# Kernel optimization log

Hardware: AMD Instinct MI355X
Metric: run time of the kernel (lower is better)

## Reference

```python
import jax, jax.numpy as jnp
import numpy as np

S, F, K, D, H, DT = 64, 10, 7, 512, 14, 128


def _mlp(x, W1, b1, W2, b2, g, b):
    # Linear(512,128) -> ReLU -> Linear(128,128) -> BatchNorm1d(128) (eval mode = affine)
    h = jax.nn.relu(x @ W1 + b1)
    y = h @ W2 + b2
    return y * g + b


def setup_inputs() -> dict:
    key = jax.random.key(0)
    ks = jax.random.split(key, 10)
    rng = np.random.default_rng(0)
    # per-(seg,class) random frame permutation and random class picks (torch.randperm / randint)
    perm_idx = jnp.asarray(np.argsort(rng.random((S, K, F)), axis=-1), jnp.int32)
    cls_idx = jnp.asarray(rng.integers(0, K, (S, K, F)), jnp.int32)
    sc = 0.02
    return {
        "feat_a": jax.random.normal(ks[0], (S, K, D), jnp.float32),
        "pred_a": jax.random.uniform(ks[1], (S, K), jnp.float32),
        "feat_v_raw": jax.random.normal(ks[2], (S * F, D, H, H), jnp.float32),
        "pred_v": jax.random.normal(ks[3], (S * F, K), jnp.float32),
        "cam": jax.random.uniform(ks[4], (S * F, K, H, H), jnp.float32),
        "W1a": jax.random.normal(ks[5], (D, DT), jnp.float32) * sc,
        "b1a": jnp.zeros((DT,), jnp.float32),
        "W2a": jax.random.normal(ks[6], (DT, DT), jnp.float32) * sc,
        "b2a": jnp.zeros((DT,), jnp.float32),
        "ga": jnp.ones((DT,), jnp.float32),
        "bna": jnp.zeros((DT,), jnp.float32),
        "W1v": jax.random.normal(ks[7], (D, DT), jnp.float32) * sc,
        "b1v": jnp.zeros((DT,), jnp.float32),
        "W2v": jax.random.normal(ks[8], (DT, DT), jnp.float32) * sc,
        "b2v": jnp.zeros((DT,), jnp.float32),
        "gv": jnp.ones((DT,), jnp.float32),
        "bnv": jnp.zeros((DT,), jnp.float32),
        "perm_idx": perm_idx,
        "cls_idx": cls_idx,
    }


def reference(feat_a, pred_a, feat_v_raw, pred_v, cam,
              W1a, b1a, W2a, b2a, ga, bna,
              W1v, b1v, W2v, b2v, gv, bnv,
              perm_idx, cls_idx):
    # cam-weighted foreground pooling (cam_pool fg branch), contracted so the
    # [N,K,D,HW] intermediate is never materialized
    cam_sum = jnp.sum(cam, axis=(-2, -1)) + 1e-10            # [N,K]
    fg = jnp.einsum('nchw,nkhw->nkc', feat_v_raw, cam) / cam_sum[..., None]
    feat_v = fg.reshape(S, F, K, D)                           # [S,F,K,D]

    pv = jax.nn.sigmoid(pred_v).reshape(S, F, K)              # index_v

    Ta = _mlp(feat_a, W1a, b1a, W2a, b2a, ga, bna)            # [S,K,DT]
    Tv = _mlp(feat_v, W1v, b1v, W2v, b2v, gv, bnv)            # [S,F,K,DT]

    # 'same' pairs: (seg, class k, frame f) with pred_a>0.3 and sigmoid(pred_v)>0.3
    Tvt = jnp.transpose(Tv, (0, 2, 1, 3))                     # [S,K,F,DT]
    loss_co = jnp.mean((Ta[:, :, None, :] - Tvt) ** 2, -1)    # [S,K,F]

    # 'differ' pairs: partner segment rank = seg^1, random frame perm + random class,
    # first num = floor(pred_a*F) entries kept
    rank = jnp.arange(S) ^ 1
    Tv_d = Tv[rank[:, None, None], perm_idx, cls_idx]         # [S,K,F,DT]
    loss_di = jnp.mean((Ta[:, :, None, :] - Tv_d) ** 2, -1)   # [S,K,F]

    act_a = pred_a > 0.3                                      # index_a
    num = jnp.floor(pred_a * F).astype(jnp.int32)
    mask_co = act_a[:, :, None] & (jnp.transpose(pv, (0, 2, 1)) > 0.3)
    mask_di = act_a[:, :, None] & (jnp.arange(F)[None, None, :] < num[:, :, None])

    losses = jnp.stack([loss_co * mask_co, loss_di * mask_di], 0)  # [2,S,K,F]
    return losses, mask_co, mask_di
```

## Files before the change

kernel.cpp:

```cpp
#include <hip/hip_runtime.h>
#include <hip/hip_bf16.h>
#include <math.h>

#define S 64
#define F 10
#define K 7
#define D 512
#define HH 196
#define DT 128
#define NF (S*F)
#define NROWS_V (S*F*K)
#define NROWS_A (S*K)
#define NOUT (S*K*F)
#define MLP_R 8
#define NA_BLK (NROWS_A / MLP_R)
#define NV_BLK (NROWS_V / MLP_R)
#define WT 32
#define WTILE_F4 (WT * DT / 4)

typedef short bf16x8 __attribute__((ext_vector_type(8)));
typedef float f32x4 __attribute__((ext_vector_type(4)));

__device__ __forceinline__ short bfc(float x) {
  __hip_bfloat16 h = __float2bfloat16(x);
  return *reinterpret_cast<short*>(&h);
}

__global__ __launch_bounds__(256) void fg_kernel(
    const float* __restrict__ feat, const float* __restrict__ cam,
    float* __restrict__ fg) {
  const int t = threadIdx.x;
  const int lane = t & 63;
  const int w = t >> 6;
  const int col = lane & 15;
  const int kg = lane >> 4;
  const int n = blockIdx.x >> 1;
  const int half = blockIdx.x & 1;
  const int c0blk = half * 256;

  const float* featn = feat + ((size_t)n * D + c0blk) * HH;
  const float* camn = cam + (size_t)n * K * HH;

  bf16x8 bs[7];
  {
    const float* crow = camn + col * HH;
#pragma unroll
    for (int s = 0; s < 7; ++s) {
      float v0 = 0.f, v1 = 0.f, v2 = 0.f, v3 = 0.f;
      float v4 = 0.f, v5 = 0.f, v6 = 0.f, v7 = 0.f;
      if (col < 7) {
        if (s < 6) {
          const float4 lo = *reinterpret_cast<const float4*>(crow + s * 32 + kg * 8);
          const float4 hi = *reinterpret_cast<const float4*>(crow + s * 32 + kg * 8 + 4);
          v0 = lo.x; v1 = lo.y; v2 = lo.z; v3 = lo.w;
          v4 = hi.x; v5 = hi.y; v6 = hi.z; v7 = hi.w;
        } else if (kg == 0) {
          const float4 lo = *reinterpret_cast<const float4*>(crow + 192);
          v0 = lo.x; v1 = lo.y; v2 = lo.z; v3 = lo.w;
        }
      }
      bs[s][0] = bfc(v0); bs[s][1] = bfc(v1); bs[s][2] = bfc(v2); bs[s][3] = bfc(v3);
      bs[s][4] = bfc(v4); bs[s][5] = bfc(v5); bs[s][6] = bfc(v6); bs[s][7] = bfc(v7);
    }
  }

  float invc = 0.f;
#pragma unroll
  for (int k = 0; k < K; ++k) {
    float4 cv = (lane < 49)
                    ? *reinterpret_cast<const float4*>(camn + k * HH + 4 * lane)
                    : make_float4(0.f, 0.f, 0.f, 0.f);
    float s = cv.x + cv.y + cv.z + cv.w;
#pragma unroll
    for (int m = 32; m >= 1; m >>= 1) s += __shfl_xor(s, m, 64);
    const float iv = 1.0f / (s + 1e-10f);
    if (col == k) invc = iv;
  }

  float* fgn = fg + (size_t)n * K * D;

#pragma unroll
  for (int mt = 0; mt < 4; ++mt) {
    const int chl = (w * 4 + mt) * 16 + col;
    const float* rowp = featn + (size_t)chl * HH;

    f32x4 acc = {0.f, 0.f, 0.f, 0.f};
#pragma unroll
    for (int s = 0; s < 7; ++s) {
      float v0 = 0.f, v1 = 0.f, v2 = 0.f, v3 = 0.f;
      float v4 = 0.f, v5 = 0.f, v6 = 0.f, v7 = 0.f;
      if (s < 6) {
        const float4 lo = *reinterpret_cast<const float4*>(rowp + s * 32 + kg * 8);
        const float4 hi = *reinterpret_cast<const float4*>(rowp + s * 32 + kg * 8 + 4);
        v0 = lo.x; v1 = lo.y; v2 = lo.z; v3 = lo.w;
        v4 = hi.x; v5 = hi.y; v6 = hi.z; v7 = hi.w;
      } else if (kg == 0) {
        const float4 lo = *reinterpret_cast<const float4*>(rowp + 192);
        v0 = lo.x; v1 = lo.y; v2 = lo.z; v3 = lo.w;
      }
      bf16x8 a;
      a[0] = bfc(v0); a[1] = bfc(v1); a[2] = bfc(v2); a[3] = bfc(v3);
      a[4] = bfc(v4); a[5] = bfc(v5); a[6] = bfc(v6); a[7] = bfc(v7);
      acc = __builtin_amdgcn_mfma_f32_16x16x32_bf16(a, bs[s], acc, 0, 0, 0);
    }

    if (col < 7) {
      float4 o;
      o.x = acc[0] * invc; o.y = acc[1] * invc;
      o.z = acc[2] * invc; o.w = acc[3] * invc;
      *reinterpret_cast<float4*>(
          fgn + (size_t)col * D + c0blk + (w * 4 + mt) * 16 + kg * 4) = o;
    }
  }
}

__device__ __forceinline__ void fma4(float4& acc, float sx, const float4& wv) {
  acc.x += sx * wv.x; acc.y += sx * wv.y; acc.z += sx * wv.z; acc.w += sx * wv.w;
}

__device__ __forceinline__ void stage_w(const float* src, float4* dst, int t) {
#pragma unroll
  for (int i = 0; i < WTILE_F4; i += 256) {
    __builtin_amdgcn_global_load_lds(
        (const __attribute__((address_space(1))) void*)(src + (size_t)(i + t) * 4),
        (__attribute__((address_space(3))) void*)(dst + i + t), 16, 0, 0);
  }
}

__global__ __launch_bounds__(256) void mlp2_kernel(
    const float* __restrict__ Xa, const float* __restrict__ Xv,
    const float* __restrict__ W1a, const float* __restrict__ b1a,
    const float* __restrict__ W2a, const float* __restrict__ b2a,
    const float* __restrict__ ga, const float* __restrict__ bna,
    const float* __restrict__ W1v, const float* __restrict__ b1v,
    const float* __restrict__ W2v, const float* __restrict__ b2v,
    const float* __restrict__ gv, const float* __restrict__ bnv,
    float* __restrict__ Ta, float* __restrict__ Tv) {
  __shared__ float4 wbuf[2][WTILE_F4];
  __shared__ float hs[MLP_R * DT];
  const int t = threadIdx.x;
  const int b = blockIdx.x;

  const float *X, *W1, *b1, *W2, *b2, *g, *bn;
  float* out;
  int r0;
  if (b < NA_BLK) {
    X = Xa; W1 = W1a; b1 = b1a; W2 = W2a; b2 = b2a; g = ga; bn = bna;
    out = Ta; r0 = b * MLP_R;
  } else {
    X = Xv; W1 = W1v; b1 = b1v; W2 = W2v; b2 = b2v; g = gv; bn = bnv;
    out = Tv; r0 = (b - NA_BLK) * MLP_R;
  }

  const int cg = t & 31;
  const int j0 = cg * 4;
  const int rp = t >> 5;
  const float4* xrow = reinterpret_cast<const float4*>(X + (size_t)(r0 + rp) * D);

  stage_w(W1, &wbuf[0][0], t);
  __syncthreads();

  float4 a0 = *reinterpret_cast<const float4*>(b1 + j0);
  for (int dt = 0; dt < 16; ++dt) {
    if (dt < 15) stage_w(W1 + (size_t)(dt + 1) * WT * DT, &wbuf[(dt + 1) & 1][0], t);
    else         stage_w(W2, &wbuf[0][0], t);
    const float4* wb = &wbuf[dt & 1][0];
#pragma unroll
    for (int d4 = 0; d4 < 8; ++d4) {
      const float4 x0 = xrow[dt * 8 + d4];
      const float4 w0 = wb[(d4 * 4 + 0) * 32 + cg];
      const float4 w1 = wb[(d4 * 4 + 1) * 32 + cg];
      const float4 w2 = wb[(d4 * 4 + 2) * 32 + cg];
      const float4 w3 = wb[(d4 * 4 + 3) * 32 + cg];
      fma4(a0, x0.x, w0); fma4(a0, x0.y, w1); fma4(a0, x0.z, w2); fma4(a0, x0.w, w3);
    }
    __syncthreads();
  }

  a0.x = fmaxf(a0.x, 0.f); a0.y = fmaxf(a0.y, 0.f);
  a0.z = fmaxf(a0.z, 0.f); a0.w = fmaxf(a0.w, 0.f);
  *reinterpret_cast<float4*>(hs + rp * DT + j0) = a0;
  __syncthreads();

  const float4* hrow = reinterpret_cast<const float4*>(hs + rp * DT);

  float4 c0 = *reinterpret_cast<const float4*>(b2 + j0);
  for (int dt = 0; dt < 4; ++dt) {
    if (dt < 3) stage_w(W2 + (size_t)(dt + 1) * WT * DT, &wbuf[(dt + 1) & 1][0], t);
    const float4* wb = &wbuf[dt & 1][0];
#pragma unroll
    for (int d4 = 0; d4 < 8; ++d4) {
      const float4 x0 = hrow[dt * 8 + d4];
      const float4 w0 = wb[(d4 * 4 + 0) * 32 + cg];
      const float4 w1 = wb[(d4 * 4 + 1) * 32 + cg];
      const float4 w2 = wb[(d4 * 4 + 2) * 32 + cg];
      const float4 w3 = wb[(d4 * 4 + 3) * 32 + cg];
      fma4(c0, x0.x, w0); fma4(c0, x0.y, w1); fma4(c0, x0.z, w2); fma4(c0, x0.w, w3);
    }
    __syncthreads();
  }

  const float4 gvv = *reinterpret_cast<const float4*>(g + j0);
  const float4 bv = *reinterpret_cast<const float4*>(bn + j0);
  float4 o0;
  o0.x = c0.x * gvv.x + bv.x; o0.y = c0.y * gvv.y + bv.y;
  o0.z = c0.z * gvv.z + bv.z; o0.w = c0.w * gvv.w + bv.w;
  *reinterpret_cast<float4*>(out + (size_t)(r0 + rp) * DT + j0) = o0;
}

__global__ __launch_bounds__(256) void loss_kernel(
    const float* __restrict__ Ta, const float* __restrict__ Tv,
    const float* __restrict__ pred_a, const float* __restrict__ pred_v,
    const int* __restrict__ perm_idx, const int* __restrict__ cls_idx,
    float* __restrict__ out) {
  const int t = threadIdx.x;
  const int sub = t & 31;
  const int idx = blockIdx.x * 8 + (t >> 5);
  const int f = idx % F;
  const int k = (idx / F) % K;
  const int s = idx / (K * F);

  const int p = perm_idx[idx];
  const int c = cls_idx[idx];
  const int rowd = ((s ^ 1) * F + p) * K + c;

  float4 ta = reinterpret_cast<const float4*>(Ta)[(s * K + k) * 32 + sub];
  float4 tv = reinterpret_cast<const float4*>(Tv)[((s * F + f) * K + k) * 32 + sub];
  float4 td = reinterpret_cast<const float4*>(Tv)[rowd * 32 + sub];
  float d1 = 0.f, d2 = 0.f, e;
  e = ta.x - tv.x; d1 += e * e;
  e = ta.y - tv.y; d1 += e * e;
  e = ta.z - tv.z; d1 += e * e;
  e = ta.w - tv.w; d1 += e * e;
  e = ta.x - td.x; d2 += e * e;
  e = ta.y - td.y; d2 += e * e;
  e = ta.z - td.z; d2 += e * e;
  e = ta.w - td.w; d2 += e * e;
#pragma unroll
  for (int m = 16; m >= 1; m >>= 1) {
    d1 += __shfl_xor(d1, m, 64);
    d2 += __shfl_xor(d2, m, 64);
  }
  if (sub == 0) {
    float pa = pred_a[s * K + k];
    bool act = pa > 0.3f;
    int num = (int)floorf(pa * (float)F);
    float pvv = pred_v[(s * F + f) * K + k];
    float sg = 1.0f / (1.0f + expf(-pvv));
    bool mco = act && (sg > 0.3f);
    bool mdi = act && (f < num);
    float lco = d1 * (1.0f / 128.0f);
    float ldi = d2 * (1.0f / 128.0f);
    out[idx] = mco ? lco : 0.0f;
    out[NOUT + idx] = mdi ? ldi : 0.0f;
    out[2 * NOUT + idx] = mco ? 1.0f : 0.0f;
    out[3 * NOUT + idx] = mdi ? 1.0f : 0.0f;
  }
}

extern "C" void kernel_launch(void* const* d_in, const int* in_sizes, int n_in,
                              void* d_out, int out_size, void* d_ws, size_t ws_size,
                              hipStream_t stream) {
  const float* feat_a     = (const float*)d_in[0];
  const float* pred_a     = (const float*)d_in[1];
  const float* feat_v_raw = (const float*)d_in[2];
  const float* pred_v     = (const float*)d_in[3];
  const float* cam        = (const float*)d_in[4];
  const float* W1a = (const float*)d_in[5];
  const float* b1a = (const float*)d_in[6];
  const float* W2a = (const float*)d_in[7];
  const float* b2a = (const float*)d_in[8];
  const float* ga  = (const float*)d_in[9];
  const float* bna = (const float*)d_in[10];
  const float* W1v = (const float*)d_in[11];
  const float* b1v = (const float*)d_in[12];
  const float* W2v = (const float*)d_in[13];
  const float* b2v = (const float*)d_in[14];
  const float* gv  = (const float*)d_in[15];
  const float* bnv = (const float*)d_in[16];
  const int* perm_idx = (const int*)d_in[17];
  const int* cls_idx  = (const int*)d_in[18];
  float* out = (float*)d_out;

  float* ws = (float*)d_ws;
  float* fg = ws;
  float* Ta = fg + (size_t)NF * K * D;
  float* Tv = Ta + (size_t)NROWS_A * DT;

  fg_kernel<<<NF * 2, 256, 0, stream>>>(feat_v_raw, cam, fg);
  mlp2_kernel<<<NA_BLK + NV_BLK, 256, 0, stream>>>(
      feat_a, fg, W1a, b1a, W2a, b2a, ga, bna,
      W1v, b1v, W2v, b2v, gv, bnv, Ta, Tv);
  loss_kernel<<<NOUT / 8, 256, 0, stream>>>(Ta, Tv, pred_a, pred_v, perm_idx,
                                            cls_idx, out);
}
```

Measured before the change: 82.53 us.

## Run projection MLPs on bf16 MFMA with pre-transposed bf16 weights

Swaps the fp32 FMA MLP kernel, which staged weights through LDS, for an MFMA-based kernel working on 16-row tiles with bf16 inputs. A new conversion kernel casts feat_a to bf16 and transposes and casts the weight matrices each call. fg_kernel now writes its pooled features as bf16, which halves that intermediate's traffic. This adds an extra launch and lowers precision for the MLP inputs and hidden activations.

```diff
diff --git a/kernel.cpp b/kernel.cpp
--- a/kernel.cpp
+++ b/kernel.cpp
@@ -12,23 +12,56 @@
 #define NROWS_V (S*F*K)
 #define NROWS_A (S*K)
 #define NOUT (S*K*F)
-#define MLP_R 8
-#define NA_BLK (NROWS_A / MLP_R)
-#define NV_BLK (NROWS_V / MLP_R)
-#define WT 32
-#define WTILE_F4 (WT * DT / 4)
+#define MLP_BLK_A (NROWS_A / 16)
+#define MLP_BLK_V (NROWS_V / 16)
 
 typedef short bf16x8 __attribute__((ext_vector_type(8)));
 typedef float f32x4 __attribute__((ext_vector_type(4)));
 
-__device__ __forceinline__ short bfc(float x) {
+__device__ __forceinline__ unsigned short bfc(float x) {
   __hip_bfloat16 h = __float2bfloat16(x);
-  return *reinterpret_cast<short*>(&h);
+  return *reinterpret_cast<unsigned short*>(&h);
+}
+
+__global__ __launch_bounds__(256) void conv_kernel(
+    const float* __restrict__ feat_a,
+    const float* __restrict__ W1a, const float* __restrict__ W1v,
+    const float* __restrict__ W2a, const float* __restrict__ W2v,
+    unsigned short* __restrict__ XaB,
+    unsigned short* __restrict__ W1aT, unsigned short* __restrict__ W1vT,
+    unsigned short* __restrict__ W2aT, unsigned short* __restrict__ W2vT) {
+  const int b = blockIdx.x;
+  const int t = threadIdx.x;
+  if (b < 224) {
+    const int o = b * 256 + t;
+    const float4 v = reinterpret_cast<const float4*>(feat_a)[o];
+    unsigned short s0 = bfc(v.x), s1 = bfc(v.y), s2 = bfc(v.z), s3 = bfc(v.w);
+    uint2 pk;
+    pk.x = ((unsigned)s1 << 16) | s0;
+    pk.y = ((unsigned)s3 << 16) | s2;
+    reinterpret_cast<uint2*>(XaB)[o] = pk;
+  } else if (b < 480) {
+    const int o = (b - 224) * 256 + t;
+    const int j = o >> 9, d = o & 511;
+    W1aT[o] = bfc(W1a[d * DT + j]);
+  } else if (b < 736) {
+    const int o = (b - 480) * 256 + t;
+    const int j = o >> 9, d = o & 511;
+    W1vT[o] = bfc(W1v[d * DT + j]);
+  } else if (b < 800) {
+    const int o = (b - 736) * 256 + t;
+    const int j = o >> 7, d = o & 127;
+    W2aT[o] = bfc(W2a[d * DT + j]);
+  } else {
+    const int o = (b - 800) * 256 + t;
+    const int j = o >> 7, d = o & 127;
+    W2vT[o] = bfc(W2v[d * DT + j]);
+  }
 }
 
 __global__ __launch_bounds__(256) void fg_kernel(
     const float* __restrict__ feat, const float* __restrict__ cam,
-    float* __restrict__ fg) {
+    unsigned short* __restrict__ fgb) {
   const int t = threadIdx.x;
   const int lane = t & 63;
   const int w = t >> 6;
@@ -77,7 +110,7 @@
     if (col == k) invc = iv;
   }
 
-  float* fgn = fg + (size_t)n * K * D;
+  unsigned short* fgn = fgb + (size_t)n * K * D;
 
 #pragma unroll
   for (int mt = 0; mt < 4; ++mt) {
@@ -105,107 +138,99 @@
     }
 
     if (col < 7) {
-      float4 o;
-      o.x = acc[0] * invc; o.y = acc[1] * invc;
-      o.z = acc[2] * invc; o.w = acc[3] * invc;
-      *reinterpret_cast<float4*>(
-          fgn + (size_t)col * D + c0blk + (w * 4 + mt) * 16 + kg * 4) = o;
-    }
-  }
-}
-
-__device__ __forceinline__ void fma4(float4& acc, float sx, const float4& wv) {
-  acc.x += sx * wv.x; acc.y += sx * wv.y; acc.z += sx * wv.z; acc.w += sx * wv.w;
-}
-
-__device__ __forceinline__ void stage_w(const float* src, float4* dst, int t) {
-#pragma unroll
-  for (int i = 0; i < WTILE_F4; i += 256) {
-    __builtin_amdgcn_global_load_lds(
-        (const __attribute__((address_space(1))) void*)(src + (size_t)(i + t) * 4),
-        (__attribute__((address_space(3))) void*)(dst + i + t), 16, 0, 0);
-  }
-}
-
-__global__ __launch_bounds__(256) void mlp2_kernel(
-    const float* __restrict__ Xa, const float* __restrict__ Xv,
-    const float* __restrict__ W1a, const float* __restrict__ b1a,
-    const float* __restrict__ W2a, const float* __restrict__ b2a,
+      uint2 pk;
+      pk.x = ((unsigned)bfc(acc[1] * invc) << 16) | bfc(acc[0] * invc);
+      pk.y = ((unsigned)bfc(acc[3] * invc) << 16) | bfc(acc[2] * invc);
+      *reinterpret_cast<uint2*>(
+          fgn + (size_t)col * D + c0blk + (w * 4 + mt) * 16 + kg * 4) = pk;
+    }
+  }
+}
+
+__global__ __launch_bounds__(256) void mlp3_kernel(
+    const unsigned short* __restrict__ XaB, const unsigned short* __restrict__ XvB,
+    const unsigned short* __restrict__ W1aT, const unsigned short* __restrict__ W2aT,
+    const float* __restrict__ b1a, const float* __restrict__ b2a,
     const float* __restrict__ ga, const float* __restrict__ bna,
-    const float* __restrict__ W1v, const float* __restrict__ b1v,
-    const float* __restrict__ W2v, const float* __restrict__ b2v,
+    const unsigned short* __restrict__ W1vT, const unsigned short* __restrict__ W2vT,
+    const float* __restrict__ b1v, const float* __restrict__ b2v,
     const float* __restrict__ gv, const float* __restrict__ bnv,
     float* __restrict__ Ta, float* __restrict__ Tv) {
-  __shared__ float4 wbuf[2][WTILE_F4];
-  __shared__ float hs[MLP_R * DT];
+  __shared__ unsigned short hs[16 * 144];
+
   const int t = threadIdx.x;
+  const int lane = t & 63;
+  const int w = t >> 6;
+  const int c15 = lane & 15;
+  const int kg = lane >> 4;
+  const int nbase = w * 32;
   const int b = blockIdx.x;
 
-  const float *X, *W1, *b1, *W2, *b2, *g, *bn;
+  const unsigned short *XB, *W1T, *W2T;
+  const float *b1, *b2, *g, *bn;
   float* out;
   int r0;
-  if (b < NA_BLK) {
-    X = Xa; W1 = W1a; b1 = b1a; W2 = W2a; b2 = b2a; g = ga; bn = bna;
-    out = Ta; r0 = b * MLP_R;
+  if (b < MLP_BLK_A) {
+    XB = XaB; W1T = W1aT; W2T = W2aT; b1 = b1a; b2 = b2a; g = ga; bn = bna;
+    out = Ta; r0 = b * 16;
   } else {
-    X = Xv; W1 = W1v; b1 = b1v; W2 = W2v; b2 = b2v; g = gv; bn = bnv;
-    out = Tv; r0 = (b - NA_BLK) * MLP_R;
-  }
-
-  const int cg = t & 31;
-  const int j0 = cg * 4;
-  const int rp = t >> 5;
-  const float4* xrow = reinterpret_cast<const float4*>(X + (size_t)(r0 + rp) * D);
-
-  stage_w(W1, &wbuf[0][0], t);
+    XB = XvB; W1T = W1vT; W2T = W2vT; b1 = b1v; b2 = b2v; g = gv; bn = bnv;
+    out = Tv; r0 = (b - MLP_BLK_A) * 16;
+  }
+
+  const unsigned short* xp = XB + (size_t)(r0 + c15) * D + kg * 8;
+  const unsigned short* wp0 = W1T + (size_t)(nbase + c15) * D + kg * 8;
+  const unsigned short* wp1 = W1T + (size_t)(nbase + 16 + c15) * D + kg * 8;
+
+  f32x4 acc0 = {0.f, 0.f, 0.f, 0.f};
+  f32x4 acc1 = {0.f, 0.f, 0.f, 0.f};
+#pragma unroll
+  for (int s = 0; s < 16; ++s) {
+    const bf16x8 a = *reinterpret_cast<const bf16x8*>(xp + s * 32);
+    const bf16x8 w0 = *reinterpret_cast<const bf16x8*>(wp0 + s * 32);
+    const bf16x8 w1 = *reinterpret_cast<const bf16x8*>(wp1 + s * 32);
+    acc0 = __builtin_amdgcn_mfma_f32_16x16x32_bf16(a, w0, acc0, 0, 0, 0);
+    acc1 = __builtin_amdgcn_mfma_f32_16x16x32_bf16(a, w1, acc1, 0, 0, 0);
+  }
+
+  {
+    const float bc0 = b1[nbase + c15];
+    const float bc1 = b1[nbase + 16 + c15];
+#pragma unroll
+    for (int i = 0; i < 4; ++i) {
+      const int row = kg * 4 + i;
+      hs[row * 144 + nbase + c15] = bfc(fmaxf(acc0[i] + bc0, 0.f));
+      hs[row * 144 + nbase + 16 + c15] = bfc(fmaxf(acc1[i] + bc1, 0.f));
+    }
+  }
   __syncthreads();
 
-  float4 a0 = *reinterpret_cast<const float4*>(b1 + j0);
-  for (int dt = 0; dt < 16; ++dt) {
-    if (dt < 15) stage_w(W1 + (size_t)(dt + 1) * WT * DT, &wbuf[(dt + 1) & 1][0], t);
-    else         stage_w(W2, &wbuf[0][0], t);
-    const float4* wb = &wbuf[dt & 1][0];
-#pragma unroll
-    for (int d4 = 0; d4 < 8; ++d4) {
-      const float4 x0 = xrow[dt * 8 + d4];
-      const float4 w0 = wb[(d4 * 4 + 0) * 32 + cg];
-      const float4 w1 = wb[(d4 * 4 + 1) * 32 + cg];
-      const float4 w2 = wb[(d4 * 4 + 2) * 32 + cg];
-      const float4 w3 = wb[(d4 * 4 + 3) * 32 + cg];
-      fma4(a0, x0.x, w0); fma4(a0, x0.y, w1); fma4(a0, x0.z, w2); fma4(a0, x0.w, w3);
-    }
-    __syncthreads();
-  }
-
-  a0.x = fmaxf(a0.x, 0.f); a0.y = fmaxf(a0.y, 0.f);
-  a0.z = fmaxf(a0.z, 0.f); a0.w = fmaxf(a0.w, 0.f);
-  *reinterpret_cast<float4*>(hs + rp * DT + j0) = a0;
-  __syncthreads();
-
-  const float4* hrow = reinterpret_cast<const float4*>(hs + rp * DT);
-
-  float4 c0 = *reinterpret_cast<const float4*>(b2 + j0);
-  for (int dt = 0; dt < 4; ++dt) {
-    if (dt < 3) stage_w(W2 + (size_t)(dt + 1) * WT * DT, &wbuf[(dt + 1) & 1][0], t);
-    const float4* wb = &wbuf[dt & 1][0];
-#pragma unroll
-    for (int d4 = 0; d4 < 8; ++d4) {
-      const float4 x0 = hrow[dt * 8 + d4];
-      const float4 w0 = wb[(d4 * 4 + 0) * 32 + cg];
-      const float4 w1 = wb[(d4 * 4 + 1) * 32 + cg];
-      const float4 w2 = wb[(d4 * 4 + 2) * 32 + cg];
-      const float4 w3 = wb[(d4 * 4 + 3) * 32 + cg];
-      fma4(c0, x0.x, w0); fma4(c0, x0.y, w1); fma4(c0, x0.z, w2); fma4(c0, x0.w, w3);
-    }
-    __syncthreads();
-  }
-
-  const float4 gvv = *reinterpret_cast<const float4*>(g + j0);
-  const float4 bv = *reinterpret_cast<const float4*>(bn + j0);
-  float4 o0;
-  o0.x = c0.x * gvv.x + bv.x; o0.y = c0.y * gvv.y + bv.y;
-  o0.z = c0.z * gvv.z + bv.z; o0.w = c0.w * gvv.w + bv.w;
-  *reinterpret_cast<float4*>(out + (size_t)(r0 + rp) * DT + j0) = o0;
+  const unsigned short* w2p0 = W2T + (size_t)(nbase + c15) * DT + kg * 8;
+  const unsigned short* w2p1 = W2T + (size_t)(nbase + 16 + c15) * DT + kg * 8;
+  f32x4 c0 = {0.f, 0.f, 0.f, 0.f};
+  f32x4 c1 = {0.f, 0.f, 0.f, 0.f};
+#pragma unroll
+  for (int s = 0; s < 4; ++s) {
+    const bf16x8 a = *reinterpret_cast<const bf16x8*>(hs + c15 * 144 + s * 32 + kg * 8);
+    const bf16x8 w0 = *reinterpret_cast<const bf16x8*>(w2p0 + s * 32);
+    const bf16x8 w1 = *reinterpret_cast<const bf16x8*>(w2p1 + s * 32);
+    c0 = __builtin_amdgcn_mfma_f32_16x16x32_bf16(a, w0, c0, 0, 0, 0);
+    c1 = __builtin_amdgcn_mfma_f32_16x16x32_bf16(a, w1, c1, 0, 0, 0);
+  }
+
+  {
+    const int col0 = nbase + c15;
+    const int col1 = nbase + 16 + c15;
+    const float b20 = b2[col0], b21 = b2[col1];
+    const float g0 = g[col0], g1 = g[col1];
+    const float n0 = bn[col0], n1 = bn[col1];
+#pragma unroll
+    for (int i = 0; i < 4; ++i) {
+      const int row = r0 + kg * 4 + i;
+      out[(size_t)row * DT + col0] = (c0[i] + b20) * g0 + n0;
+      out[(size_t)row * DT + col1] = (c1[i] + b21) * g1 + n1;
+    }
+  }
 }
 
 __global__ __launch_bounds__(256) void loss_kernel(
@@ -282,15 +307,22 @@
   const int* cls_idx  = (const int*)d_in[18];
   float* out = (float*)d_out;
 
-  float* ws = (float*)d_ws;
-  float* fg = ws;
-  float* Ta = fg + (size_t)NF * K * D;
-  float* Tv = Ta + (size_t)NROWS_A * DT;
-
-  fg_kernel<<<NF * 2, 256, 0, stream>>>(feat_v_raw, cam, fg);
-  mlp2_kernel<<<NA_BLK + NV_BLK, 256, 0, stream>>>(
-      feat_a, fg, W1a, b1a, W2a, b2a, ga, bna,
-      W1v, b1v, W2v, b2v, gv, bnv, Ta, Tv);
+  char* w = (char*)d_ws;
+  unsigned short* fgb  = (unsigned short*)(w);
+  unsigned short* XaB  = (unsigned short*)(w + 4587520);
+  unsigned short* W1aT = (unsigned short*)(w + 4587520 + 458752);
+  unsigned short* W1vT = (unsigned short*)(w + 4587520 + 458752 + 131072);
+  unsigned short* W2aT = (unsigned short*)(w + 4587520 + 458752 + 262144);
+  unsigned short* W2vT = (unsigned short*)(w + 4587520 + 458752 + 262144 + 32768);
+  float* Ta = (float*)(w + 4587520 + 458752 + 262144 + 65536);
+  float* Tv = (float*)(w + 4587520 + 458752 + 262144 + 65536 + 229376);
+
+  conv_kernel<<<864, 256, 0, stream>>>(feat_a, W1a, W1v, W2a, W2v,
+                                       XaB, W1aT, W1vT, W2aT, W2vT);
+  fg_kernel<<<NF * 2, 256, 0, stream>>>(feat_v_raw, cam, fgb);
+  mlp3_kernel<<<MLP_BLK_A + MLP_BLK_V, 256, 0, stream>>>(
+      XaB, fgb, W1aT, W2aT, b1a, b2a, ga, bna,
+      W1vT, W2vT, b1v, b2v, gv, bnv, Ta, Tv);
   loss_kernel<<<NOUT / 8, 256, 0, stream>>>(Ta, Tv, pred_a, pred_v, perm_idx,
                                             cls_idx, out);
 }
```

Result: faster. 71.63 us (-13.2%).
